# Kernel tuning notes

Hardware: AMD Instinct MI355X
Metric: run time of the kernel (lower is better)

## Reference

```python
import jax, jax.numpy as jnp
import numpy as np

B, N, D = 8, 2048, 256

def setup_inputs() -> dict:
    key = jax.random.key(0)
    ks = jax.random.split(key, 8)
    sc = 1.0 / np.sqrt(D)
    return {
        "x": jax.random.normal(ks[0], (B, N, D), dtype=jnp.float32),
        "W_fp": jax.random.normal(ks[1], (D, D), dtype=jnp.float32) * sc,
        "b_fp": jnp.zeros((D,), dtype=jnp.float32),
        "w_s": jax.random.normal(ks[2], (D,), dtype=jnp.float32) * sc,
        "b_s": jnp.zeros((), dtype=jnp.float32),
        "W_rp": jax.random.normal(ks[3], (D, D), dtype=jnp.float32) * sc,
        "b_rp": jnp.zeros((D,), dtype=jnp.float32),
        "W_gp": jax.random.normal(ks[4], (D, D), dtype=jnp.float32) * sc,
        "b_gp": jnp.zeros((D,), dtype=jnp.float32),
        "gamma": jnp.ones((D,), dtype=jnp.float32),
        "beta": jnp.zeros((D,), dtype=jnp.float32),
    }

def reference(x, W_fp, b_fp, w_s, b_s, W_rp, b_rp, W_gp, b_gp, gamma, beta):
    # feature projection: [B, N, D]
    proj = jnp.einsum('bnd,de->bne', x, W_fp) + b_fp
    # F.normalize(p=2, dim=-1) with eps=1e-12
    nrm = jnp.sqrt(jnp.sum(proj * proj, axis=-1, keepdims=True))
    xn = proj / jnp.maximum(nrm, 1e-12)
    # cosine similarity matrix [B, N, N]
    sim = jnp.einsum('bnd,bmd->bnm', xn, xn)
    # adj_scaler: Linear(D,1)+sigmoid is constant along the broadcast axis ->
    # compute per-node scalar once [B, N] (same math as the O(N^2*D) expand)
    s = jax.nn.sigmoid(jnp.einsum('bnd,d->bn', proj, w_s) + b_s)
    scaler = jnp.clip(0.5 * (s[:, :, None] + s[:, None, :]), 1e-6, 1.0)
    adj = jnp.maximum(scaler * sim, 1e-6)  # clamp(min=1e-6)
    degree = jnp.maximum(jnp.sum(adj, axis=2, keepdims=True), 1e-6)
    norm_adj = adj / degree
    # aggregation + region projection
    region = jnp.einsum('bnm,bmd->bnd', norm_adj, proj)
    region = jnp.einsum('bnd,de->bne', region, W_rp) + b_rp
    # global pooling + projection: [B, 1, D]
    g = jnp.mean(region, axis=1, keepdims=True)
    g = jnp.einsum('bnd,de->bne', g, W_gp) + b_gp
    input_global = jnp.mean(x, axis=1, keepdims=True)
    h = g + input_global
    # LayerNorm (eps=1e-5)
    mu = jnp.mean(h, axis=-1, keepdims=True)
    var = jnp.mean((h - mu) ** 2, axis=-1, keepdims=True)
    out = (h - mu) / jnp.sqrt(var + 1e-5) * gamma + beta
    return out, adj
```

## Files before the change

### kernel.cpp

```cpp
#include <hip/hip_runtime.h>
#include <hip/hip_bf16.h>
#include <math.h>

#define Bn 8
#define Nn 2048
#define Dn 256

typedef short short8 __attribute__((ext_vector_type(8)));
typedef float floatx4 __attribute__((ext_vector_type(4)));

__device__ __forceinline__ short f2bf_bits(float f) {
    __bf16 h = (__bf16)f;
    return __builtin_bit_cast(short, h);
}

__device__ __forceinline__ float bf2f(short s) {
    unsigned u = ((unsigned)(unsigned short)s) << 16;
    return __builtin_bit_cast(float, u);
}

__device__ __forceinline__ void gl_lds16(const void* gsrc, void* ldst) {
    __builtin_amdgcn_global_load_lds(
        (const __attribute__((address_space(1))) void*)gsrc,
        (__attribute__((address_space(3))) void*)ldst, 16, 0, 0);
}

__device__ __forceinline__ float sigmoidf_(float z) {
    return 1.0f / (1.0f + __expf(-z));
}


__global__ __launch_bounds__(256) void k_transpose(const float* __restrict__ W,
                                                   short* __restrict__ Wt) {
    __shared__ float Ts[64][65];
    const int t = threadIdx.x;
    const int dt0 = blockIdx.x * 64, et0 = blockIdx.y * 64;
    const int ro = t >> 4, co = (t & 15) * 4;
    #pragma unroll
    for (int rr = 0; rr < 4; ++rr) {
        int row = rr * 16 + ro;
        float4 v = *(const float4*)(W + (size_t)(dt0 + row) * Dn + et0 + co);
        Ts[row][co + 0] = v.x; Ts[row][co + 1] = v.y;
        Ts[row][co + 2] = v.z; Ts[row][co + 3] = v.w;
    }
    __syncthreads();
    const int e = t >> 2, cd0 = (t & 3) * 16;
    short8 a, b;
    #pragma unroll
    for (int i = 0; i < 8; ++i) {
        a[i] = f2bf_bits(Ts[cd0 + i][e]);
        b[i] = f2bf_bits(Ts[cd0 + 8 + i][e]);
    }
    *(short8*)(Wt + (size_t)(et0 + e) * Dn + dt0 + cd0) = a;
    *(short8*)(Wt + (size_t)(et0 + e) * Dn + dt0 + cd0 + 8) = b;
}


__global__ __launch_bounds__(512) void k_projxn(
    const float* __restrict__ x, const short* __restrict__ Wt,
    const float* __restrict__ b_fp, const float* __restrict__ w_s,
    short* __restrict__ xn, float* __restrict__ sdot, float* __restrict__ nrm,
    float* __restrict__ xpart) {
    __shared__ __align__(16) short As[64 * 64];
    __shared__ __align__(16) short Bs[256 * 64];
    __shared__ float xsumS[8 * 256];
    __shared__ float redW[2][64];
    __shared__ float redN[2][64];
    const int t = threadIdx.x;
    const int bm = blockIdx.x * 64;
    const int lane = t & 63, wv = t >> 6;
    const int wm = (wv & 3) * 16;
    const int jh = wv >> 2;
    const int l15 = lane & 15, q = lane >> 4;

    for (int i = t; i < 2048; i += 512) xsumS[i] = 0.f;

    floatx4 acc[8];
    #pragma unroll
    for (int j = 0; j < 8; ++j) acc[j] = (floatx4){0.f, 0.f, 0.f, 0.f};

    const int rA = t >> 3, cA = (t & 7) * 8;
    const int rB = t >> 3, cB = (t & 7) * 8;

    for (int k0 = 0; k0 < Dn; k0 += 64) {
        const float* gp = x + (size_t)(bm + rA) * Dn + k0 + cA;
        float4 v0 = *(const float4*)gp;
        float4 v1 = *(const float4*)(gp + 4);
        short8 o0;
        o0[0] = f2bf_bits(v0.x); o0[1] = f2bf_bits(v0.y);
        o0[2] = f2bf_bits(v0.z); o0[3] = f2bf_bits(v0.w);
        o0[4] = f2bf_bits(v1.x); o0[5] = f2bf_bits(v1.y);
        o0[6] = f2bf_bits(v1.z); o0[7] = f2bf_bits(v1.w);
        *(short8*)(As + rA * 64 + cA) = o0;
        #pragma unroll
        for (int cc = 0; cc < 4; ++cc)
            gl_lds16(Wt + (size_t)(cc * 64 + rB) * Dn + k0 + cB,
                     Bs + (cc * 64 + rB) * 64 + cB);
        __syncthreads();
        #pragma unroll
        for (int ks = 0; ks < 2; ++ks) {
            short8 af = *(const short8*)(As + (wm + l15) * 64 + ks * 32 + q * 8);
            #pragma unroll
            for (int jj = 0; jj < 8; ++jj) {
                short8 bfr = *(const short8*)(Bs + (jh * 128 + jj * 16 + l15) * 64 + ks * 32 + q * 8);
                acc[jj] = __builtin_amdgcn_mfma_f32_16x16x32_bf16(af, bfr, acc[jj], 0, 0, 0);
            }
        }
        {
            float s = 0.f;
            #pragma unroll
            for (int r = 0; r < 8; ++r)
                s += bf2f(As[(wv * 8 + r) * 64 + lane]);
            xsumS[wv * 256 + k0 + lane] += s;
        }
        __syncthreads();
    }
    if (t < 256) {
        float xs = 0.f;
        #pragma unroll
        for (int w = 0; w < 8; ++w) xs += xsumS[w * 256 + t];
        xpart[(size_t)blockIdx.x * Dn + t] = xs;
    }
    float bfv[8], wsv[8];
    #pragma unroll
    for (int jj = 0; jj < 8; ++jj) {
        bfv[jj] = b_fp[jh * 128 + jj * 16 + l15];
        wsv[jj] = w_s[jh * 128 + jj * 16 + l15];
    }
    float vv[4][8];
    #pragma unroll
    for (int reg = 0; reg < 4; ++reg) {
        float pw = 0.f, pn = 0.f;
        #pragma unroll
        for (int jj = 0; jj < 8; ++jj) {
            float v = acc[jj][reg] + bfv[jj];
            vv[reg][jj] = v;
            pw += v * wsv[jj];
            pn += v * v;
        }
        #pragma unroll
        for (int m = 1; m < 16; m <<= 1) {
            pw += __shfl_xor(pw, m);
            pn += __shfl_xor(pn, m);
        }
        if (l15 == 0) {
            redW[jh][wm + q * 4 + reg] = pw;
            redN[jh][wm + q * 4 + reg] = pn;
        }
    }
    __syncthreads();
    #pragma unroll
    for (int reg = 0; reg < 4; ++reg) {
        int lr = wm + q * 4 + reg;
        float pw = redW[0][lr] + redW[1][lr];
        float pn = redN[0][lr] + redN[1][lr];
        float nc = fmaxf(sqrtf(pn), 1e-12f);
        float inv = 1.0f / nc;
        int row = bm + lr;
        size_t rbase = (size_t)row * Dn + jh * 128 + l15;
        #pragma unroll
        for (int jj = 0; jj < 8; ++jj)
            xn[rbase + jj * 16] = f2bf_bits(vv[reg][jj] * inv);
        if (jh == 0 && l15 == 0) {
            sdot[row] = pw;
            nrm[row] = nc;
        }
    }
}


__global__ __launch_bounds__(256) void k_sim(
    const short* __restrict__ xn, const float* __restrict__ sdot,
    const float* __restrict__ b_s, float* __restrict__ adj,
    float* __restrict__ deg_part) {
    __shared__ __align__(16) short As[128 * 64];
    __shared__ __align__(16) short Bs[128 * 64];
    __shared__ float degS[2][128];
    const int t = threadIdx.x;
    int lin = (blockIdx.z * 16 + blockIdx.y) * 16 + blockIdx.x;
    const int b = lin & 7;
    const int pos = lin >> 3;
    const int by = pos >> 4, cx = pos & 15;
    const int bn = cx * 128;
    const int bm = by * 128;
    const int lane = t & 63, wv = t >> 6;
    const int wm = (wv >> 1) * 64, wn = (wv & 1) * 64;
    const int l15 = lane & 15, q4 = lane >> 4;
    const int rr = t >> 3, c8 = (t & 7) * 8;
    const short* xb = xn + (size_t)b * Nn * Dn;

    floatx4 acc[4][4];
    #pragma unroll
    for (int i = 0; i < 4; ++i)
        #pragma unroll
        for (int j = 0; j < 4; ++j) acc[i][j] = (floatx4){0.f, 0.f, 0.f, 0.f};

    for (int k0 = 0; k0 < Dn; k0 += 64) {
        #pragma unroll
        for (int cc = 0; cc < 4; ++cc) {
            int r = cc * 32 + rr;
            gl_lds16(xb + (size_t)(bm + r) * Dn + k0 + c8, As + r * 64 + c8);
            gl_lds16(xb + (size_t)(bn + r) * Dn + k0 + c8, Bs + r * 64 + c8);
        }
        __syncthreads();
        #pragma unroll
        for (int ks = 0; ks < 2; ++ks) {
            short8 af[4], bfr[4];
            #pragma unroll
            for (int i = 0; i < 4; ++i)
                af[i] = *(const short8*)(As + (wm + i * 16 + l15) * 64 + ks * 32 + q4 * 8);
            #pragma unroll
            for (int j = 0; j < 4; ++j)
                bfr[j] = *(const short8*)(Bs + (wn + j * 16 + l15) * 64 + ks * 32 + q4 * 8);
            #pragma unroll
            for (int i = 0; i < 4; ++i)
                #pragma unroll
                for (int j = 0; j < 4; ++j)
                    acc[i][j] = __builtin_amdgcn_mfma_f32_16x16x32_bf16(bfr[j], af[i], acc[i][j], 0, 0, 0);
        }
        __syncthreads();
    }
    const float bsv = b_s[0];
    float srow[4];
    #pragma unroll
    for (int i = 0; i < 4; ++i)
        srow[i] = sigmoidf_(sdot[b * Nn + bm + wm + i * 16 + l15] + bsv);
    float scol[4][4];
    #pragma unroll
    for (int j = 0; j < 4; ++j)
        #pragma unroll
        for (int reg = 0; reg < 4; ++reg)
            scol[j][reg] = sigmoidf_(sdot[b * Nn + bn + wn + j * 16 + q4 * 4 + reg] + bsv);
    #pragma unroll
    for (int i = 0; i < 4; ++i) {
        float rs = 0.f;
        size_t rbase = ((size_t)b * Nn + (bm + wm + i * 16 + l15)) * Nn + bn + wn + q4 * 4;
        #pragma unroll
        for (int j = 0; j < 4; ++j) {
            float4 o;
            float sc;
            sc = fminf(fmaxf(0.5f * (srow[i] + scol[j][0]), 1e-6f), 1.0f);
            o.x = fmaxf(sc * acc[i][j][0], 1e-6f);
            sc = fminf(fmaxf(0.5f * (srow[i] + scol[j][1]), 1e-6f), 1.0f);
            o.y = fmaxf(sc * acc[i][j][1], 1e-6f);
            sc = fminf(fmaxf(0.5f * (srow[i] + scol[j][2]), 1e-6f), 1.0f);
            o.z = fmaxf(sc * acc[i][j][2], 1e-6f);
            sc = fminf(fmaxf(0.5f * (srow[i] + scol[j][3]), 1e-6f), 1.0f);
            o.w = fmaxf(sc * acc[i][j][3], 1e-6f);
            *(float4*)(adj + rbase + (size_t)j * 16) = o;
            rs += o.x + o.y + o.z + o.w;
        }
        rs += __shfl_xor(rs, 16);
        rs += __shfl_xor(rs, 32);
        if (q4 == 0) degS[wv & 1][wm + i * 16 + l15] = rs;
    }
    __syncthreads();
    if (t < 128)
        deg_part[((size_t)(b * 16 + cx)) * Nn + bm + t] = degS[0][t] + degS[1][t];
}


__global__ __launch_bounds__(1024) void k_colsum(
    const float* __restrict__ adj, const float* __restrict__ deg_part,
    const short* __restrict__ xn, const float* __restrict__ nrm,
    float* __restrict__ gpart) {
    int b = blockIdx.x, ck = blockIdx.y, t = threadIdx.x;
    __shared__ float invdeg[Nn];
    __shared__ float part[64][64];
    __shared__ float csL[64];
    __shared__ float gQ[4][Dn];
    #pragma unroll
    for (int rc = 0; rc < 2; ++rc) {
        int row = rc * 1024 + t;
        float s = 0.f;
        #pragma unroll
        for (int cx = 0; cx < 16; ++cx)
            s += deg_part[((size_t)(b * 16 + cx)) * Nn + row];
        invdeg[row] = 1.0f / fmaxf(s, 1e-6f);
    }
    __syncthreads();
    const int lc = (t & 15) * 4;
    const int rg = t >> 4;
    const int c0 = ck * 64;
    float sx = 0.f, sy = 0.f, sz = 0.f, sw = 0.f;
    for (int r = rg; r < Nn; r += 64) {
        float4 v = *(const float4*)(adj + ((size_t)b * Nn + r) * Nn + c0 + lc);
        float w = invdeg[r];
        sx += v.x * w; sy += v.y * w; sz += v.z * w; sw += v.w * w;
    }
    part[rg][lc + 0] = sx; part[rg][lc + 1] = sy;
    part[rg][lc + 2] = sz; part[rg][lc + 3] = sw;
    __syncthreads();
    if (t < 64) {
        float s = 0.f;
        #pragma unroll
        for (int g = 0; g < 64; ++g) s += part[g][t];
        csL[t] = s * nrm[b * Nn + c0 + t];
    }
    __syncthreads();
    {
        int h = t >> 8, d = t & 255;
        float g = 0.f;
        #pragma unroll 4
        for (int mi = 0; mi < 16; ++mi) {
            int m = h * 16 + mi;
            g += csL[m] * bf2f(xn[((size_t)(b * Nn + c0 + m)) * Dn + d]);
        }
        gQ[h][d] = g;
    }
    __syncthreads();
    if (t < Dn)
        gpart[(b * 32 + ck) * Dn + t] = gQ[0][t] + gQ[1][t] + gQ[2][t] + gQ[3][t];
}


__global__ __launch_bounds__(1024) void k_final2(
    const float* __restrict__ gpart, const float* __restrict__ xpart,
    const float* __restrict__ W_rp, const float* __restrict__ b_rp,
    const float* __restrict__ W_gp, const float* __restrict__ b_gp,
    const float* __restrict__ gamma, const float* __restrict__ beta,
    float* __restrict__ out) {
    int b = blockIdx.x, t = threadIdx.x;
    const int d = t & 255, c4 = t >> 8;
    __shared__ float pS[4][Dn];
    __shared__ float xS[4][Dn];
    __shared__ float gp_s[Dn];
    __shared__ float xm_s[Dn];
    __shared__ float g1_s[Dn];
    __shared__ float red[8];
    {
        float gs = 0.f, xs = 0.f;
        #pragma unroll
        for (int k = 0; k < 8; ++k) {
            int ck = c4 * 8 + k;
            gs += gpart[(b * 32 + ck) * Dn + d];
            xs += xpart[(b * 32 + ck) * Dn + d];
        }
        pS[c4][d] = gs;
        xS[c4][d] = xs;
    }
    __syncthreads();
    if (t < Dn) {
        gp_s[t] = (pS[0][t] + pS[1][t] + pS[2][t] + pS[3][t]) * (1.0f / Nn);
        xm_s[t] = (xS[0][t] + xS[1][t] + xS[2][t] + xS[3][t]) * (1.0f / Nn);
    }
    __syncthreads();
    {
        float m1 = 0.f;
        #pragma unroll 4
        for (int i = 0; i < 64; ++i) {
            int dd = c4 * 64 + i;
            m1 += gp_s[dd] * W_rp[dd * Dn + d];
        }
        pS[c4][d] = m1;
    }
    __syncthreads();
    if (t < Dn) g1_s[t] = b_rp[t] + pS[0][t] + pS[1][t] + pS[2][t] + pS[3][t];
    __syncthreads();
    {
        float m2 = 0.f;
        #pragma unroll 4
        for (int i = 0; i < 64; ++i) {
            int ee = c4 * 64 + i;
            m2 += g1_s[ee] * W_gp[ee * Dn + d];
        }
        pS[c4][d] = m2;
    }
    __syncthreads();
    float h = 0.f;
    if (t < Dn) {
        h = b_gp[t] + pS[0][t] + pS[1][t] + pS[2][t] + pS[3][t] + xm_s[t];
        float sum = h;
        #pragma unroll
        for (int m = 1; m < 64; m <<= 1) sum += __shfl_xor(sum, m);
        if ((t & 63) == 0) red[t >> 6] = sum;
    }
    __syncthreads();
    float mu = (red[0] + red[1] + red[2] + red[3]) * (1.0f / Dn);
    if (t < Dn) {
        float dv = h - mu;
        float s2 = dv * dv;
        #pragma unroll
        for (int m = 1; m < 64; m <<= 1) s2 += __shfl_xor(s2, m);
        if ((t & 63) == 0) red[4 + (t >> 6)] = s2;
    }
    __syncthreads();
    if (t < Dn) {
        float dv = h - mu;
        float var = (red[4] + red[5] + red[6] + red[7]) * (1.0f / Dn);
        out[b * Dn + t] = dv * rsqrtf(var + 1e-5f) * gamma[t] + beta[t];
    }
}


extern "C" void kernel_launch(void* const* d_in, const int* in_sizes, int n_in,
                              void* d_out, int out_size, void* d_ws, size_t ws_size,
                              hipStream_t stream) {
    const float* x     = (const float*)d_in[0];
    const float* W_fp  = (const float*)d_in[1];
    const float* b_fp  = (const float*)d_in[2];
    const float* w_s   = (const float*)d_in[3];
    const float* b_s   = (const float*)d_in[4];
    const float* W_rp  = (const float*)d_in[5];
    const float* b_rp  = (const float*)d_in[6];
    const float* W_gp  = (const float*)d_in[7];
    const float* b_gp  = (const float*)d_in[8];
    const float* gamma = (const float*)d_in[9];
    const float* beta  = (const float*)d_in[10];

    float* out = (float*)d_out;
    float* adj = out + Bn * Dn;

    char* ws = (char*)d_ws;
    short* xn    = (short*)(ws);
    short* Wt    = (short*)(ws + 8388608);
    float* sdot  = (float*)(ws + 8519680);
    float* nrm   = (float*)(ws + 8585216);
    float* degp  = (float*)(ws + 8650752);
    float* gpart = (float*)(ws + 9699328);
    float* xpart = (float*)(ws + 9961472);

    k_transpose<<<dim3(4, 4), 256, 0, stream>>>(W_fp, Wt);
    k_projxn<<<(Bn * Nn) / 64, 512, 0, stream>>>(x, Wt, b_fp, w_s, xn, sdot, nrm, xpart);
    k_sim<<<dim3(Nn / 128, Nn / 128, Bn), 256, 0, stream>>>(xn, sdot, b_s, adj, degp);
    k_colsum<<<dim3(Bn, 32), 1024, 0, stream>>>(adj, degp, xn, nrm, gpart);
    k_final2<<<Bn, 1024, 0, stream>>>(gpart, xpart, W_rp, b_rp, W_gp, b_gp, gamma, beta, out);
}
```

Baseline: 238.4 us.

## Widen k_sim tile to 128x256 with 512 threads and split degree reduction kernel

```diff
diff --git a/kernel.cpp b/kernel.cpp
--- a/kernel.cpp
+++ b/kernel.cpp
@@ -169,22 +169,23 @@
 }
 
 
-__global__ __launch_bounds__(256) void k_sim(
+__global__ __launch_bounds__(512) void k_sim(
     const short* __restrict__ xn, const float* __restrict__ sdot,
     const float* __restrict__ b_s, float* __restrict__ adj,
     float* __restrict__ deg_part) {
     __shared__ __align__(16) short As[128 * 64];
-    __shared__ __align__(16) short Bs[128 * 64];
-    __shared__ float degS[2][128];
+    __shared__ __align__(16) short Bs[256 * 64];
+    __shared__ float degS[4][128];
     const int t = threadIdx.x;
-    int lin = (blockIdx.z * 16 + blockIdx.y) * 16 + blockIdx.x;
+    int lin = (blockIdx.z * 16 + blockIdx.y) * 8 + blockIdx.x;
     const int b = lin & 7;
     const int pos = lin >> 3;
-    const int by = pos >> 4, cx = pos & 15;
-    const int bn = cx * 128;
+    const int by = pos >> 3, cx = pos & 7;
     const int bm = by * 128;
+    const int bn = cx * 256;
     const int lane = t & 63, wv = t >> 6;
-    const int wm = (wv >> 1) * 64, wn = (wv & 1) * 64;
+    const int wm = (wv >> 2) * 64;
+    const int wn = (wv & 3) * 64;
     const int l15 = lane & 15, q4 = lane >> 4;
     const int rr = t >> 3, c8 = (t & 7) * 8;
     const short* xb = xn + (size_t)b * Nn * Dn;
@@ -197,9 +198,13 @@
 
     for (int k0 = 0; k0 < Dn; k0 += 64) {
         #pragma unroll
+        for (int cc = 0; cc < 2; ++cc) {
+            int r = cc * 64 + rr;
+            gl_lds16(xb + (size_t)(bm + r) * Dn + k0 + c8, As + r * 64 + c8);
+        }
+        #pragma unroll
         for (int cc = 0; cc < 4; ++cc) {
-            int r = cc * 32 + rr;
-            gl_lds16(xb + (size_t)(bm + r) * Dn + k0 + c8, As + r * 64 + c8);
+            int r = cc * 64 + rr;
             gl_lds16(xb + (size_t)(bn + r) * Dn + k0 + c8, Bs + r * 64 + c8);
         }
         __syncthreads();
@@ -252,32 +257,37 @@
         }
         rs += __shfl_xor(rs, 16);
         rs += __shfl_xor(rs, 32);
-        if (q4 == 0) degS[wv & 1][wm + i * 16 + l15] = rs;
+        if (q4 == 0) degS[wv & 3][wm + i * 16 + l15] = rs;
     }
     __syncthreads();
     if (t < 128)
-        deg_part[((size_t)(b * 16 + cx)) * Nn + bm + t] = degS[0][t] + degS[1][t];
+        deg_part[((size_t)(b * 8 + cx)) * Nn + bm + t] =
+            degS[0][t] + degS[1][t] + degS[2][t] + degS[3][t];
+}
+
+
+__global__ __launch_bounds__(256) void k_deg(const float* __restrict__ deg_part,
+                                             float* __restrict__ invdeg) {
+    int b = blockIdx.x, t = blockIdx.y * 256 + threadIdx.x;
+    float s = 0.f;
+    #pragma unroll
+    for (int cx = 0; cx < 8; ++cx)
+        s += deg_part[((size_t)(b * 8 + cx)) * Nn + t];
+    invdeg[b * Nn + t] = 1.0f / fmaxf(s, 1e-6f);
 }
 
 
 __global__ __launch_bounds__(1024) void k_colsum(
-    const float* __restrict__ adj, const float* __restrict__ deg_part,
+    const float* __restrict__ adj, const float* __restrict__ invdeg,
     const short* __restrict__ xn, const float* __restrict__ nrm,
     float* __restrict__ gpart) {
     int b = blockIdx.x, ck = blockIdx.y, t = threadIdx.x;
-    __shared__ float invdeg[Nn];
+    __shared__ float invS[Nn];
     __shared__ float part[64][64];
     __shared__ float csL[64];
     __shared__ float gQ[4][Dn];
-    #pragma unroll
-    for (int rc = 0; rc < 2; ++rc) {
-        int row = rc * 1024 + t;
-        float s = 0.f;
-        #pragma unroll
-        for (int cx = 0; cx < 16; ++cx)
-            s += deg_part[((size_t)(b * 16 + cx)) * Nn + row];
-        invdeg[row] = 1.0f / fmaxf(s, 1e-6f);
-    }
+    invS[t] = invdeg[b * Nn + t];
+    invS[t + 1024] = invdeg[b * Nn + t + 1024];
     __syncthreads();
     const int lc = (t & 15) * 4;
     const int rg = t >> 4;
@@ -285,7 +295,7 @@
     float sx = 0.f, sy = 0.f, sz = 0.f, sw = 0.f;
     for (int r = rg; r < Nn; r += 64) {
         float4 v = *(const float4*)(adj + ((size_t)b * Nn + r) * Nn + c0 + lc);
-        float w = invdeg[r];
+        float w = invS[r];
         sx += v.x * w; sy += v.y * w; sz += v.z * w; sw += v.w * w;
     }
     part[rg][lc + 0] = sx; part[rg][lc + 1] = sy;
@@ -412,17 +422,19 @@
     float* adj = out + Bn * Dn;
 
     char* ws = (char*)d_ws;
-    short* xn    = (short*)(ws);
-    short* Wt    = (short*)(ws + 8388608);
-    float* sdot  = (float*)(ws + 8519680);
-    float* nrm   = (float*)(ws + 8585216);
-    float* degp  = (float*)(ws + 8650752);
-    float* gpart = (float*)(ws + 9699328);
-    float* xpart = (float*)(ws + 9961472);
+    short* xn     = (short*)(ws);
+    short* Wt     = (short*)(ws + 8388608);
+    float* sdot   = (float*)(ws + 8519680);
+    float* nrm    = (float*)(ws + 8585216);
+    float* degp   = (float*)(ws + 8650752);
+    float* invdeg = (float*)(ws + 9175040);
+    float* gpart  = (float*)(ws + 9699328);
+    float* xpart  = (float*)(ws + 9961472);
 
     k_transpose<<<dim3(4, 4), 256, 0, stream>>>(W_fp, Wt);
     k_projxn<<<(Bn * Nn) / 64, 512, 0, stream>>>(x, Wt, b_fp, w_s, xn, sdot, nrm, xpart);
-    k_sim<<<dim3(Nn / 128, Nn / 128, Bn), 256, 0, stream>>>(xn, sdot, b_s, adj, degp);
-    k_colsum<<<dim3(Bn, 32), 1024, 0, stream>>>(adj, degp, xn, nrm, gpart);
+    k_sim<<<dim3(8, 16, 8), 512, 0, stream>>>(xn, sdot, b_s, adj, degp);
+    k_deg<<<dim3(Bn, 8), 256, 0, stream>>>(degp, invdeg);
+    k_colsum<<<dim3(Bn, 32), 1024, 0, stream>>>(adj, invdeg, xn, nrm, gpart);
     k_final2<<<Bn, 1024, 0, stream>>>(gpart, xpart, W_rp, b_rp, W_gp, b_gp, gamma, beta, out);
 }
```

Measured after the change: 237.8 us, median of 2. No clear change (-0.3%).
